# Kernel optimization log

Measured on AMD Instinct MI355X. Metric: run time of the kernel, lower is better.

Reference implementation:

```python
import jax, jax.numpy as jnp
import numpy as np

INT8_MAX = 127.0

def _quant_ste(x, axis):
    """Dynamic symmetric int8 fake-quant along `axis` (per-channel scales).
    Returns dequantized values; math matches int8 dot * scales (AQT-style)."""
    amax = jnp.max(jnp.abs(x), axis=axis, keepdims=True)
    scale = jnp.maximum(amax, 1e-6) / INT8_MAX
    q = jnp.clip(jnp.round(x / scale), -INT8_MAX, INT8_MAX)
    return q * scale

def setup_inputs() -> dict:
    key = jax.random.key(0)
    k1, k2 = jax.random.split(key)
    inputs = jax.random.normal(k1, (4, 2048, 4096), dtype=jnp.float32)
    kernel = jax.random.normal(k2, (4096, 4096), dtype=jnp.float32) * 0.02
    return {"inputs": inputs, "kernel": kernel}

def reference(inputs, kernel):
    # eqn: '...y,yz->...z' with quantized dot_general:
    # per-row (last-axis) dynamic int8 quant of activations,
    # per-output-column int8 quant of kernel, int8 matmul, dequant by scales.
    xq = _quant_ste(inputs, axis=-1)   # [B, S, D]
    kq = _quant_ste(kernel, axis=0)    # [D, F]
    return jnp.einsum('bsd,df->bsf', xq, kq)  # [B, S, F]
```

## Files before the change

kernel.cpp:

```cpp
#include <hip/hip_runtime.h>


#define M_DIM 8192
#define K_DIM 4096
#define N_DIM 4096

typedef int v4i __attribute__((ext_vector_type(4)));
typedef __attribute__((address_space(3))) void lds_void_t;
typedef const __attribute__((address_space(1))) void g_void_t;

__global__ void quant_act(const float* __restrict__ X,
                          signed char* __restrict__ At,
                          float* __restrict__ sx) {
  const int row = blockIdx.x;
  const int t = threadIdx.x;
  const float* xr = X + (size_t)row * K_DIM;
  float4 v[4];
  float am = 0.f;
#pragma unroll
  for (int c = 0; c < 4; ++c) {
    v[c] = ((const float4*)xr)[c * 256 + t];
    am = fmaxf(am, fmaxf(fmaxf(fabsf(v[c].x), fabsf(v[c].y)),
                         fmaxf(fabsf(v[c].z), fabsf(v[c].w))));
  }
#pragma unroll
  for (int off = 32; off > 0; off >>= 1)
    am = fmaxf(am, __shfl_down(am, off));
  __shared__ float red[4];
  __shared__ float s_inv;
  __shared__ unsigned int shuf[1024];
  if ((t & 63) == 0) red[t >> 6] = am;
  __syncthreads();
  if (t == 0) {
    float m = fmaxf(fmaxf(red[0], red[1]), fmaxf(red[2], red[3]));
    float scale = fmaxf(m, 1e-6f) / 127.0f;
    sx[row] = scale;
    s_inv = 1.0f / scale;
  }
  __syncthreads();
  const float inv = s_inv;
#pragma unroll
  for (int c = 0; c < 4; ++c) {
    int q0 = (int)fminf(fmaxf(rintf(v[c].x * inv), -127.f), 127.f);
    int q1 = (int)fminf(fmaxf(rintf(v[c].y * inv), -127.f), 127.f);
    int q2 = (int)fminf(fmaxf(rintf(v[c].z * inv), -127.f), 127.f);
    int q3 = (int)fminf(fmaxf(rintf(v[c].w * inv), -127.f), 127.f);
    shuf[c * 256 + t] = (q0 & 255) | ((q1 & 255) << 8) | ((q2 & 255) << 16) | (q3 << 24);
  }
  __syncthreads();
  v4i w = *(const v4i*)&shuf[t * 4];
  signed char* dst = At + (size_t)(row >> 4) * 65536 + t * 256 + (row & 15) * 16;
  *(v4i*)dst = w;
}

__global__ void wk_amax_part(const float* __restrict__ Kmat, float* __restrict__ part) {
  const int f = blockIdx.x * 256 + threadIdx.x;
  const float* p = Kmat + (size_t)(blockIdx.y * 128) * N_DIM + f;
  float a0 = 0.f, a1 = 0.f, a2 = 0.f, a3 = 0.f;
#pragma unroll 4
  for (int i = 0; i < 32; ++i) {
    a0 = fmaxf(a0, fabsf(p[0 * N_DIM]));
    a1 = fmaxf(a1, fabsf(p[1 * N_DIM]));
    a2 = fmaxf(a2, fabsf(p[2 * N_DIM]));
    a3 = fmaxf(a3, fabsf(p[3 * N_DIM]));
    p += 4 * N_DIM;
  }
  part[(size_t)blockIdx.y * N_DIM + f] = fmaxf(fmaxf(a0, a1), fmaxf(a2, a3));
}

__global__ void wk_amax_comb(const float* __restrict__ part,
                             float* __restrict__ sk, float* __restrict__ skinv) {
  const int f = blockIdx.x * 256 + threadIdx.x;
  float am = 0.f;
#pragma unroll
  for (int s = 0; s < 32; ++s) am = fmaxf(am, part[(size_t)s * N_DIM + f]);
  float scale = fmaxf(am, 1e-6f) / 127.0f;
  sk[f] = scale;
  skinv[f] = 1.0f / scale;
}

__global__ void wk_quant(const float* __restrict__ Kmat,
                         const float* __restrict__ skinv,
                         signed char* __restrict__ Bt) {
  const int f0 = (blockIdx.x & 63) * 64;
  const int d0 = (blockIdx.x >> 6) * 64;
  const int t = threadIdx.x;
  const int fl = t & 63;
  const int dl0 = t >> 6;
  __shared__ __align__(16) signed char tile[64 * 80];
  const float inv = skinv[f0 + fl];
#pragma unroll
  for (int c = 0; c < 16; ++c) {
    const int dl = c * 4 + dl0;
    float vv = Kmat[(size_t)(d0 + dl) * N_DIM + f0 + fl];
    float q = fminf(fmaxf(rintf(vv * inv), -127.f), 127.f);
    tile[fl * 80 + dl] = (signed char)(int)q;
  }
  __syncthreads();
  const int frow = t >> 2;
  const int ksl = t & 3;
  v4i w = *(const v4i*)&tile[frow * 80 + ksl * 16];
  const int f = f0 + frow;
  signed char* dst = Bt + (size_t)(f >> 4) * 65536 + ((d0 >> 4) + ksl) * 256 + (f & 15) * 16;
  *(v4i*)dst = w;
}

__global__ __launch_bounds__(256, 2) void gemm_i8(
    const signed char* __restrict__ At, const signed char* __restrict__ Bt,
    const float* __restrict__ sx, const float* __restrict__ sk,
    float* __restrict__ C) {
  const int n0 = blockIdx.x * 128;
  const int m0 = blockIdx.y * 128;
  const int t = threadIdx.x;
  const int lane = t & 63;
  const int wave = t >> 6;
  const int wm = (wave >> 1) * 64;
  const int wn = (wave & 1) * 64;
  const int lrow = lane & 15;
  const int lq = lane >> 4;

  __shared__ __align__(16) signed char lds[32768];
  signed char* lA = lds;
  signed char* lB = lds + 16384;

  v4i acc[4][4];
#pragma unroll
  for (int i = 0; i < 4; ++i)
#pragma unroll
    for (int j = 0; j < 4; ++j) acc[i][j] = (v4i){0, 0, 0, 0};

  const signed char* Abase = At + (size_t)(m0 >> 4) * 65536;
  const signed char* Bbase = Bt + (size_t)(n0 >> 4) * 65536;

  const int la = ((wave >> 1) * 4) * 2048 + lane * 16;
  const int lb = ((wave & 1) * 4) * 2048 + lane * 16;

  for (int kb = 0; kb < K_DIM; kb += 128) {
    const int kofs = kb * 16;
#pragma unroll
    for (int j = 0; j < 4; ++j) {
      const int c = j * 256 + t;
      const int mt_i = c >> 7;
      const int inner = c & 127;
      __builtin_amdgcn_global_load_lds(
          (g_void_t*)(Abase + (size_t)mt_i * 65536 + kofs + inner * 16),
          (lds_void_t*)(lA + c * 16), 16, 0, 0);
      __builtin_amdgcn_global_load_lds(
          (g_void_t*)(Bbase + (size_t)mt_i * 65536 + kofs + inner * 16),
          (lds_void_t*)(lB + c * 16), 16, 0, 0);
    }
    __syncthreads();
#pragma unroll
    for (int s = 0; s < 2; ++s) {
      v4i af[4], bf[4];
#pragma unroll
      for (int i = 0; i < 4; ++i) af[i] = *(const v4i*)(lA + la + i * 2048 + s * 1024);
#pragma unroll
      for (int i = 0; i < 4; ++i) bf[i] = *(const v4i*)(lB + lb + i * 2048 + s * 1024);
#pragma unroll
      for (int mi = 0; mi < 4; ++mi)
#pragma unroll
        for (int ni = 0; ni < 4; ++ni)
          acc[mi][ni] =
              __builtin_amdgcn_mfma_i32_16x16x64_i8(af[mi], bf[ni], acc[mi][ni], 0, 0, 0);
    }
    __syncthreads();
  }

#pragma unroll
  for (int mi = 0; mi < 4; ++mi) {
#pragma unroll
    for (int ni = 0; ni < 4; ++ni) {
      const int gn = n0 + wn + ni * 16 + lrow;
      const float skv = sk[gn];
#pragma unroll
      for (int r = 0; r < 4; ++r) {
        const int gm = m0 + wm + mi * 16 + lq * 4 + r;
        C[(size_t)gm * N_DIM + gn] = (float)acc[mi][ni][r] * sx[gm] * skv;
      }
    }
  }
}

extern "C" void kernel_launch(void* const* d_in, const int* in_sizes, int n_in,
                              void* d_out, int out_size, void* d_ws, size_t ws_size,
                              hipStream_t stream) {
  const float* X = (const float*)d_in[0];
  const float* W = (const float*)d_in[1];
  float* out = (float*)d_out;
  char* ws = (char*)d_ws;

  signed char* At = (signed char*)ws;
  signed char* Bt = (signed char*)(ws + 33554432);
  float* sx = (float*)(ws + 50331648);
  float* sk = (float*)(ws + 50364416);
  float* skinv = (float*)(ws + 50380800);
  float* part = (float*)(ws + 50397184);

  quant_act<<<M_DIM, 256, 0, stream>>>(X, At, sx);
  wk_amax_part<<<dim3(16, 32), 256, 0, stream>>>(W, part);
  wk_amax_comb<<<16, 256, 0, stream>>>(part, sk, skinv);
  wk_quant<<<4096, 256, 0, stream>>>(W, skinv, Bt);
  gemm_i8<<<dim3(N_DIM / 128, M_DIM / 128), 256, 0, stream>>>(At, Bt, sx, sk, out);
}
```

Measured before the change: 424.4 us.

## Fuse weight amax partials into activation quant kernel and drop combine launch

Merges the weight column-amax partial reduction into the activation quant kernel as 128 extra blocks, and folds the scale-combine step into wk_quant, which now also reads weights as float4. This cuts the launch count from five to three and removes one kernel's serial dependency. The int8 packed layout of A and B is also changed to 64-byte contiguous per-row chunks, with the GEMM's global-to-LDS address mapping adjusted to match. As a trade-off, each wk_quant block now recomputes the 32-way partial combine for its 64 columns.

```diff
diff --git a/kernel.cpp b/kernel.cpp
--- a/kernel.cpp
+++ b/kernel.cpp
@@ -9,11 +9,44 @@
 typedef __attribute__((address_space(3))) void lds_void_t;
 typedef const __attribute__((address_space(1))) void g_void_t;
 
-__global__ void quant_act(const float* __restrict__ X,
-                          signed char* __restrict__ At,
-                          float* __restrict__ sx) {
-  const int row = blockIdx.x;
+__global__ void fused_qa(const float* __restrict__ X,
+                         signed char* __restrict__ At,
+                         float* __restrict__ sx,
+                         const float* __restrict__ W,
+                         float* __restrict__ part) {
   const int t = threadIdx.x;
+  __shared__ float red[4];
+  __shared__ float s_inv;
+  __shared__ __align__(16) unsigned int shuf[1024];
+
+  if (blockIdx.x < 128) {
+    const int f4 = (blockIdx.x & 3) * 256 + t;
+    const int slab = blockIdx.x >> 2;
+    const float4* p = (const float4*)W + (size_t)slab * 128 * 1024 + f4;
+    float4 a0 = {0.f, 0.f, 0.f, 0.f}, a1 = {0.f, 0.f, 0.f, 0.f};
+#pragma unroll 8
+    for (int i = 0; i < 64; ++i) {
+      float4 u = p[(size_t)(2 * i) * 1024];
+      float4 v = p[(size_t)(2 * i + 1) * 1024];
+      a0.x = fmaxf(a0.x, fabsf(u.x));
+      a0.y = fmaxf(a0.y, fabsf(u.y));
+      a0.z = fmaxf(a0.z, fabsf(u.z));
+      a0.w = fmaxf(a0.w, fabsf(u.w));
+      a1.x = fmaxf(a1.x, fabsf(v.x));
+      a1.y = fmaxf(a1.y, fabsf(v.y));
+      a1.z = fmaxf(a1.z, fabsf(v.z));
+      a1.w = fmaxf(a1.w, fabsf(v.w));
+    }
+    float4 r;
+    r.x = fmaxf(a0.x, a1.x);
+    r.y = fmaxf(a0.y, a1.y);
+    r.z = fmaxf(a0.z, a1.z);
+    r.w = fmaxf(a0.w, a1.w);
+    ((float4*)part)[(size_t)slab * 1024 + f4] = r;
+    return;
+  }
+
+  const int row = blockIdx.x - 128;
   const float* xr = X + (size_t)row * K_DIM;
   float4 v[4];
   float am = 0.f;
@@ -26,9 +59,6 @@
 #pragma unroll
   for (int off = 32; off > 0; off >>= 1)
     am = fmaxf(am, __shfl_down(am, off));
-  __shared__ float red[4];
-  __shared__ float s_inv;
-  __shared__ unsigned int shuf[1024];
   if ((t & 63) == 0) red[t >> 6] = am;
   __syncthreads();
   if (t == 0) {
@@ -49,59 +79,59 @@
   }
   __syncthreads();
   v4i w = *(const v4i*)&shuf[t * 4];
-  signed char* dst = At + (size_t)(row >> 4) * 65536 + t * 256 + (row & 15) * 16;
+  signed char* dst = At + (size_t)(row >> 4) * 65536 + (t >> 2) * 1024 +
+                     (row & 15) * 64 + (t & 3) * 16;
   *(v4i*)dst = w;
 }
 
-__global__ void wk_amax_part(const float* __restrict__ Kmat, float* __restrict__ part) {
-  const int f = blockIdx.x * 256 + threadIdx.x;
-  const float* p = Kmat + (size_t)(blockIdx.y * 128) * N_DIM + f;
-  float a0 = 0.f, a1 = 0.f, a2 = 0.f, a3 = 0.f;
-#pragma unroll 4
-  for (int i = 0; i < 32; ++i) {
-    a0 = fmaxf(a0, fabsf(p[0 * N_DIM]));
-    a1 = fmaxf(a1, fabsf(p[1 * N_DIM]));
-    a2 = fmaxf(a2, fabsf(p[2 * N_DIM]));
-    a3 = fmaxf(a3, fabsf(p[3 * N_DIM]));
-    p += 4 * N_DIM;
-  }
-  part[(size_t)blockIdx.y * N_DIM + f] = fmaxf(fmaxf(a0, a1), fmaxf(a2, a3));
-}
-
-__global__ void wk_amax_comb(const float* __restrict__ part,
-                             float* __restrict__ sk, float* __restrict__ skinv) {
-  const int f = blockIdx.x * 256 + threadIdx.x;
-  float am = 0.f;
-#pragma unroll
-  for (int s = 0; s < 32; ++s) am = fmaxf(am, part[(size_t)s * N_DIM + f]);
-  float scale = fmaxf(am, 1e-6f) / 127.0f;
-  sk[f] = scale;
-  skinv[f] = 1.0f / scale;
-}
-
-__global__ void wk_quant(const float* __restrict__ Kmat,
-                         const float* __restrict__ skinv,
-                         signed char* __restrict__ Bt) {
-  const int f0 = (blockIdx.x & 63) * 64;
-  const int d0 = (blockIdx.x >> 6) * 64;
+__global__ void wk_quant(const float* __restrict__ W,
+                         const float* __restrict__ part,
+                         signed char* __restrict__ Bt,
+                         float* __restrict__ sk) {
+  const int bx = blockIdx.x;
+  const int f0 = (bx & 63) * 64;
+  const int d0 = (bx >> 6) * 64;
   const int t = threadIdx.x;
-  const int fl = t & 63;
-  const int dl0 = t >> 6;
+  const int fl4 = t & 15;
+  const int dl0 = t >> 4;
   __shared__ __align__(16) signed char tile[64 * 80];
-  const float inv = skinv[f0 + fl];
-#pragma unroll
-  for (int c = 0; c < 16; ++c) {
-    const int dl = c * 4 + dl0;
-    float vv = Kmat[(size_t)(d0 + dl) * N_DIM + f0 + fl];
-    float q = fminf(fmaxf(rintf(vv * inv), -127.f), 127.f);
-    tile[fl * 80 + dl] = (signed char)(int)q;
+  __shared__ float sl_inv[64];
+
+  float4 wv[4];
+#pragma unroll
+  for (int c = 0; c < 4; ++c) {
+    const int dl = c * 16 + dl0;
+    wv[c] = ((const float4*)W)[(size_t)(d0 + dl) * 1024 + (f0 >> 2) + fl4];
+  }
+  if (t < 64) {
+    const int f = f0 + t;
+    float m = 0.f;
+#pragma unroll
+    for (int s = 0; s < 32; ++s) m = fmaxf(m, part[(size_t)s * 4096 + f]);
+    const float scale = fmaxf(m, 1e-6f) / 127.0f;
+    if (bx < 64) sk[f] = scale;
+    sl_inv[t] = 1.0f / scale;
+  }
+  __syncthreads();
+  const float4 inv4 = *(const float4*)&sl_inv[fl4 * 4];
+#pragma unroll
+  for (int c = 0; c < 4; ++c) {
+    const int dl = c * 16 + dl0;
+    tile[(fl4 * 4 + 0) * 80 + dl] =
+        (signed char)(int)fminf(fmaxf(rintf(wv[c].x * inv4.x), -127.f), 127.f);
+    tile[(fl4 * 4 + 1) * 80 + dl] =
+        (signed char)(int)fminf(fmaxf(rintf(wv[c].y * inv4.y), -127.f), 127.f);
+    tile[(fl4 * 4 + 2) * 80 + dl] =
+        (signed char)(int)fminf(fmaxf(rintf(wv[c].z * inv4.z), -127.f), 127.f);
+    tile[(fl4 * 4 + 3) * 80 + dl] =
+        (signed char)(int)fminf(fmaxf(rintf(wv[c].w * inv4.w), -127.f), 127.f);
   }
   __syncthreads();
   const int frow = t >> 2;
   const int ksl = t & 3;
   v4i w = *(const v4i*)&tile[frow * 80 + ksl * 16];
-  const int f = f0 + frow;
-  signed char* dst = Bt + (size_t)(f >> 4) * 65536 + ((d0 >> 4) + ksl) * 256 + (f & 15) * 16;
+  signed char* dst = Bt + (size_t)((f0 + frow) >> 4) * 65536 + (d0 >> 6) * 1024 +
+                     (frow & 15) * 64 + ksl * 16;
   *(v4i*)dst = w;
 }
 
@@ -141,12 +171,12 @@
     for (int j = 0; j < 4; ++j) {
       const int c = j * 256 + t;
       const int mt_i = c >> 7;
-      const int inner = c & 127;
+      const int off = ((c >> 6) & 1) * 1024 + (c & 15) * 64 + ((c >> 4) & 3) * 16;
       __builtin_amdgcn_global_load_lds(
-          (g_void_t*)(Abase + (size_t)mt_i * 65536 + kofs + inner * 16),
+          (g_void_t*)(Abase + (size_t)mt_i * 65536 + kofs + off),
           (lds_void_t*)(lA + c * 16), 16, 0, 0);
       __builtin_amdgcn_global_load_lds(
-          (g_void_t*)(Bbase + (size_t)mt_i * 65536 + kofs + inner * 16),
+          (g_void_t*)(Bbase + (size_t)mt_i * 65536 + kofs + off),
           (lds_void_t*)(lB + c * 16), 16, 0, 0);
     }
     __syncthreads();
@@ -194,12 +224,9 @@
   signed char* Bt = (signed char*)(ws + 33554432);
   float* sx = (float*)(ws + 50331648);
   float* sk = (float*)(ws + 50364416);
-  float* skinv = (float*)(ws + 50380800);
-  float* part = (float*)(ws + 50397184);
-
-  quant_act<<<M_DIM, 256, 0, stream>>>(X, At, sx);
-  wk_amax_part<<<dim3(16, 32), 256, 0, stream>>>(W, part);
-  wk_amax_comb<<<16, 256, 0, stream>>>(part, sk, skinv);
-  wk_quant<<<4096, 256, 0, stream>>>(W, skinv, Bt);
+  float* part = (float*)(ws + 50380800);
+
+  fused_qa<<<8320, 256, 0, stream>>>(X, At, sx, W, part);
+  wk_quant<<<4096, 256, 0, stream>>>(W, part, Bt, sk);
   gemm_i8<<<dim3(N_DIM / 128, M_DIM / 128), 256, 0, stream>>>(At, Bt, sx, sk, out);
 }
```

New measurement: 432.0 us. About the same (+1.8%).
